# Kernel optimization log

Hardware: AMD Instinct MI355X
Metric: run time of the kernel (lower is better)

The kernel has to match this reference:

```python
import jax, jax.numpy as jnp
import numpy as np

USER = 100000
ITEM = 200000
N = USER + ITEM
LATDIM = 64
N_LAYERS = 3
N_EDGES = 9600000


def setup_inputs() -> dict:
    key = jax.random.key(0)
    k1, k2, k3, k4, k5 = jax.random.split(key, 5)
    # xavier_uniform for [N, latdim]: bound = sqrt(6/(fan_in+fan_out))
    bu = float(np.sqrt(6.0 / (USER + LATDIM)))
    bi = float(np.sqrt(6.0 / (ITEM + LATDIM)))
    uEmbeds = jax.random.uniform(k1, (USER, LATDIM), jnp.float32, -bu, bu)
    iEmbeds = jax.random.uniform(k2, (ITEM, LATDIM), jnp.float32, -bi, bi)
    edge_row = jax.random.randint(k3, (N_EDGES,), 0, N, dtype=jnp.int32)
    edge_col = jax.random.randint(k4, (N_EDGES,), 0, N, dtype=jnp.int32)
    edge_val = jax.random.uniform(k5, (N_EDGES,), jnp.float32) * 0.01
    return {"uEmbeds": uEmbeds, "iEmbeds": iEmbeds,
            "edge_row": edge_row, "edge_col": edge_col, "edge_val": edge_val}


def _spmm(row, col, val, x):
    # sparse adj (COO) @ dense x: gather cols, scale, scatter-add to rows
    msgs = x[col] * val[:, None]                 # [E, D]
    return jax.ops.segment_sum(msgs, row, num_segments=N)  # [N, D]


def reference(uEmbeds, iEmbeds, edge_row, edge_col, edge_val):
    # forward_gcn: multi-layer propagation, sum of all layer embeddings
    embeds = jnp.concatenate([uEmbeds, iEmbeds], axis=0)  # [N, D]
    acc = embeds
    cur = embeds
    for _ in range(N_LAYERS):
        cur = _spmm(edge_row, edge_col, edge_val, cur)
        acc = acc + cur
    return acc[:USER], acc[USER:]
```

## Files before the change

kernel.cpp:

```cpp
#include <hip/hip_runtime.h>
#include <hip/hip_bf16.h>

#define USER_N   100000
#define ITEM_N   200000
#define N_NODES  300000
#define LATDIM   64
#define N_EDGES  9600000
#define N_LAYERS 3

#define CSHIFT   11
#define CROWS    2048
#define NCOARSE  ((N_NODES + CROWS - 1) / CROWS)
#define CHUNK    4096
#define NCHUNKS  ((N_EDGES + CHUNK - 1) / CHUNK)
#define GP1      512
#define GP4      768

__device__ __forceinline__ unsigned short f2bf(float f) {
    unsigned int u = __float_as_uint(f);
    u += 0x7FFFu + ((u >> 16) & 1u);
    return (unsigned short)(u >> 16);
}
__device__ __forceinline__ float bf2f(unsigned short h) {
    return __uint_as_float(((unsigned int)h) << 16);
}

__global__ void cvt_concat_kernel(const float* __restrict__ u,
                                  const float* __restrict__ it,
                                  ushort4* __restrict__ cur0,
                                  int n4u, int n4total) {
    int stride = gridDim.x * blockDim.x;
    for (int i = blockIdx.x * blockDim.x + threadIdx.x; i < n4total; i += stride) {
        float4 v = (i < n4u) ? ((const float4*)u)[i]
                             : ((const float4*)it)[i - n4u];
        ushort4 o;
        o.x = f2bf(v.x); o.y = f2bf(v.y); o.z = f2bf(v.z); o.w = f2bf(v.w);
        cur0[i] = o;
    }
}

__global__ __launch_bounds__(256)
void p1_hist_kernel(const int* __restrict__ row, int* __restrict__ cntRaw) {
    __shared__ int h[NCOARSE];
    int t = threadIdx.x;
    for (int k = blockIdx.x; k < NCHUNKS; k += gridDim.x) {
        for (int i = t; i < NCOARSE; i += 256) h[i] = 0;
        __syncthreads();
        int e0 = k * CHUNK;
        int e1 = e0 + CHUNK; if (e1 > N_EDGES) e1 = N_EDGES;
        for (int e = e0 + t; e < e1; e += 256)
            atomicAdd(&h[row[e] >> CSHIFT], 1);
        __syncthreads();
        for (int i = t; i < NCOARSE; i += 256)
            cntRaw[i * NCHUNKS + k] = h[i];
        __syncthreads();
    }
}

__global__ __launch_bounds__(1024)
void p2_scanchunks_kernel(const int* __restrict__ cntRaw,
                          int* __restrict__ cntScan,
                          int* __restrict__ btot) {
    __shared__ int lds[1024];
    int b = blockIdx.x, t = threadIdx.x;
    const int base = t * 3;
    int v0 = 0, v1 = 0, v2 = 0;
    if (base     < NCHUNKS) v0 = cntRaw[b * NCHUNKS + base];
    if (base + 1 < NCHUNKS) v1 = cntRaw[b * NCHUNKS + base + 1];
    if (base + 2 < NCHUNKS) v2 = cntRaw[b * NCHUNKS + base + 2];
    int s = v0 + v1 + v2;
    lds[t] = s;
    __syncthreads();
    for (int off = 1; off < 1024; off <<= 1) {
        int add = (t >= off) ? lds[t - off] : 0;
        __syncthreads();
        lds[t] += add;
        __syncthreads();
    }
    int ex = lds[t] - s;
    if (base     < NCHUNKS) cntScan[b * NCHUNKS + base]     = ex;
    if (base + 1 < NCHUNKS) cntScan[b * NCHUNKS + base + 1] = ex + v0;
    if (base + 2 < NCHUNKS) cntScan[b * NCHUNKS + base + 2] = ex + v0 + v1;
    if (t == 1023) btot[b] = lds[1023];
}

__global__ void p3_scancoarse_kernel(const int* __restrict__ btot,
                                     int* __restrict__ cbase,
                                     int* __restrict__ rowPtr) {
    __shared__ int lds[256];
    int t = threadIdx.x;
    int v = (t < NCOARSE) ? btot[t] : 0;
    lds[t] = v;
    __syncthreads();
    for (int off = 1; off < 256; off <<= 1) {
        int add = (t >= off) ? lds[t - off] : 0;
        __syncthreads();
        lds[t] += add;
        __syncthreads();
    }
    if (t < NCOARSE) cbase[t] = lds[t] - v;
    if (t == NCOARSE - 1) cbase[NCOARSE] = lds[t];
    if (t == 0) rowPtr[N_NODES] = N_EDGES;
}

__global__ __launch_bounds__(256)
void p4_scatter_kernel(const int*   __restrict__ row,
                       const int*   __restrict__ col,
                       const float* __restrict__ val,
                       const int*   __restrict__ cntRaw,
                       const int*   __restrict__ cntScan,
                       const int*   __restrict__ cbase,
                       int2*        __restrict__ tempA) {
    __shared__ int2 stage[CHUNK];
    __shared__ int  dst[CHUNK];
    __shared__ int  loff[NCOARSE];
    __shared__ int  lcur[NCOARSE];
    __shared__ int  gcur[NCOARSE];
    __shared__ int  sc[256];
    int t = threadIdx.x;
    for (int k = blockIdx.x; k < NCHUNKS; k += gridDim.x) {
        int hv = 0;
        if (t < NCOARSE) {
            hv = cntRaw[t * NCHUNKS + k];
            gcur[t] = cbase[t] + cntScan[t * NCHUNKS + k];
        }
        sc[t] = hv;
        __syncthreads();
        for (int off = 1; off < 256; off <<= 1) {
            int add = (t >= off) ? sc[t - off] : 0;
            __syncthreads();
            sc[t] += add;
            __syncthreads();
        }
        if (t < NCOARSE) {
            int ex = sc[t] - hv;
            loff[t] = ex;
            lcur[t] = ex;
        }
        __syncthreads();

        int e0 = k * CHUNK;
        int e1 = e0 + CHUNK; if (e1 > N_EDGES) e1 = N_EDGES;
        int n = e1 - e0;
        for (int e = e0 + t; e < e1; e += 256) {
            int r = row[e];
            int c = r >> CSHIFT;
            int p = atomicAdd(&lcur[c], 1);
            stage[p] = make_int2(((r & (CROWS - 1)) << 19) | col[e],
                                 __float_as_int(val[e]));
            dst[p] = gcur[c] + (p - loff[c]);
        }
        __syncthreads();
        for (int j = t; j < n; j += 256)
            tempA[dst[j]] = stage[j];
        __syncthreads();
    }
}

__global__ __launch_bounds__(1024)
void passB_kernel(const int*  __restrict__ cbase,
                  const int2* __restrict__ tempA,
                  int2*       __restrict__ colval,
                  int*        __restrict__ rowPtr) {
    __shared__ int hist[CROWS];
    __shared__ int psum[1024];
    __shared__ int curs[CROWS];
    int c = blockIdx.x;
    int t = threadIdx.x;
    int beg = cbase[c], end = cbase[c + 1];

    hist[t] = 0; hist[t + 1024] = 0;
    __syncthreads();
    for (int i = beg + t; i < end; i += 1024)
        atomicAdd(&hist[((unsigned)tempA[i].x) >> 19], 1);
    __syncthreads();

    int b0 = hist[2 * t], b1 = hist[2 * t + 1];
    int tot = b0 + b1;
    psum[t] = tot;
    __syncthreads();
    for (int off = 1; off < 1024; off <<= 1) {
        int add = (t >= off) ? psum[t - off] : 0;
        __syncthreads();
        psum[t] += add;
        __syncthreads();
    }
    int ex = psum[t] - tot;
    int j0 = 2 * t, j1 = 2 * t + 1;
    int e0 = beg + ex, e1 = beg + ex + b0;
    curs[j0] = e0;
    curs[j1] = e1;
    int gr0 = c * CROWS + j0;
    int gr1 = c * CROWS + j1;
    if (gr0 < N_NODES) rowPtr[gr0] = e0;
    if (gr1 < N_NODES) rowPtr[gr1] = e1;
    __syncthreads();

    for (int i = beg + t; i < end; i += 1024) {
        int2 kv = tempA[i];
        int rl = ((unsigned)kv.x) >> 19;
        int pos = atomicAdd(&curs[rl], 1);
        colval[pos] = make_int2((kv.x & 0x7FFFF) << 4, kv.y);
    }
}

__global__ void spmm_bf16_kernel(const int*  __restrict__ rp,
                                 const int2* __restrict__ cv,
                                 const ushort4* __restrict__ x4,
                                 ushort4*       __restrict__ y4) {
    int g = (blockIdx.x * blockDim.x + threadIdx.x) >> 4;
    if (g >= N_NODES) return;
    int q = threadIdx.x & 15;
    int beg = rp[g];
    int end = rp[g + 1];
    const ushort4* xq = x4 + q;

    float s0 = 0.f, s1 = 0.f, s2 = 0.f, s3 = 0.f;
    int i = beg;
    for (; i + 8 <= end; i += 8) {
        int2 cc[8]; ushort4 gg[8];
        #pragma unroll
        for (int k = 0; k < 8; ++k) cc[k] = cv[i + k];
        #pragma unroll
        for (int k = 0; k < 8; ++k) gg[k] = xq[cc[k].x];
        #pragma unroll
        for (int k = 0; k < 8; ++k) {
            float v = __int_as_float(cc[k].y);
            s0 += bf2f(gg[k].x) * v; s1 += bf2f(gg[k].y) * v;
            s2 += bf2f(gg[k].z) * v; s3 += bf2f(gg[k].w) * v;
        }
    }
    for (; i < end; ++i) {
        int2 cc = cv[i];
        ushort4 gg = xq[cc.x];
        float v = __int_as_float(cc.y);
        s0 += bf2f(gg.x) * v; s1 += bf2f(gg.y) * v;
        s2 += bf2f(gg.z) * v; s3 += bf2f(gg.w) * v;
    }

    ushort4 o;
    o.x = f2bf(s0); o.y = f2bf(s1); o.z = f2bf(s2); o.w = f2bf(s3);
    y4[(size_t)g * 16 + q] = o;
}

__global__ void spmm_bf16_final_kernel(const int*  __restrict__ rp,
                                       const int2* __restrict__ cv,
                                       const ushort4* __restrict__ x4,
                                       const ushort4* __restrict__ c1,
                                       const float4*  __restrict__ u4,
                                       const float4*  __restrict__ i4,
                                       float4*        __restrict__ acc4) {
    int g = (blockIdx.x * blockDim.x + threadIdx.x) >> 4;
    if (g >= N_NODES) return;
    int q = threadIdx.x & 15;
    int beg = rp[g];
    int end = rp[g + 1];
    const ushort4* xq = x4 + q;

    float s0 = 0.f, s1 = 0.f, s2 = 0.f, s3 = 0.f;
    int i = beg;
    for (; i + 8 <= end; i += 8) {
        int2 cc[8]; ushort4 gg[8];
        #pragma unroll
        for (int k = 0; k < 8; ++k) cc[k] = cv[i + k];
        #pragma unroll
        for (int k = 0; k < 8; ++k) gg[k] = xq[cc[k].x];
        #pragma unroll
        for (int k = 0; k < 8; ++k) {
            float v = __int_as_float(cc[k].y);
            s0 += bf2f(gg[k].x) * v; s1 += bf2f(gg[k].y) * v;
            s2 += bf2f(gg[k].z) * v; s3 += bf2f(gg[k].w) * v;
        }
    }
    for (; i < end; ++i) {
        int2 cc = cv[i];
        ushort4 gg = xq[cc.x];
        float v = __int_as_float(cc.y);
        s0 += bf2f(gg.x) * v; s1 += bf2f(gg.y) * v;
        s2 += bf2f(gg.z) * v; s3 += bf2f(gg.w) * v;
    }

    size_t o = (size_t)g * 16 + q;
    float4 e = (g < USER_N) ? u4[o] : i4[o - (size_t)USER_N * 16];
    ushort4 a = c1[o];
    ushort4 b = x4[o];
    float4 r;
    r.x = e.x + bf2f(a.x) + bf2f(b.x) + s0;
    r.y = e.y + bf2f(a.y) + bf2f(b.y) + s1;
    r.z = e.z + bf2f(a.z) + bf2f(b.z) + s2;
    r.w = e.w + bf2f(a.w) + bf2f(b.w) + s3;
    acc4[o] = r;
}

__global__ void copy_concat_kernel(const float* __restrict__ u,
                                   const float* __restrict__ it,
                                   float* __restrict__ cur,
                                   float* __restrict__ acc,
                                   int n4u, int n4total) {
    int stride = gridDim.x * blockDim.x;
    for (int i = blockIdx.x * blockDim.x + threadIdx.x; i < n4total; i += stride) {
        float4 v = (i < n4u) ? ((const float4*)u)[i]
                             : ((const float4*)it)[i - n4u];
        ((float4*)cur)[i] = v;
        ((float4*)acc)[i] = v;
    }
}

__global__ void spmm_atomic_kernel(const int*   __restrict__ row,
                                   const int*   __restrict__ col,
                                   const float* __restrict__ val,
                                   const float* __restrict__ x,
                                   float*       __restrict__ y) {
    const int total = N_EDGES * 16;
    int stride = gridDim.x * blockDim.x;
    for (int t = blockIdx.x * blockDim.x + threadIdx.x; t < total; t += stride) {
        int e = t >> 4;
        int q = t & 15;
        int r = row[e];
        int c = col[e];
        float v = val[e];
        float4 g = ((const float4*)x)[c * 16 + q];
        float* yp = y + r * 64 + q * 4;
        atomicAdd(yp + 0, g.x * v);
        atomicAdd(yp + 1, g.y * v);
        atomicAdd(yp + 2, g.z * v);
        atomicAdd(yp + 3, g.w * v);
    }
}

__global__ void acc_add_kernel(float* __restrict__ acc,
                               const float* __restrict__ add,
                               int n4) {
    int stride = gridDim.x * blockDim.x;
    for (int i = blockIdx.x * blockDim.x + threadIdx.x; i < n4; i += stride) {
        float4 a = ((const float4*)acc)[i];
        float4 b = ((const float4*)add)[i];
        a.x += b.x; a.y += b.y; a.z += b.z; a.w += b.w;
        ((float4*)acc)[i] = a;
    }
}

extern "C" void kernel_launch(void* const* d_in, const int* in_sizes, int n_in,
                              void* d_out, int out_size, void* d_ws, size_t ws_size,
                              hipStream_t stream) {
    const float* uEmb = (const float*)d_in[0];
    const float* iEmb = (const float*)d_in[1];
    const int*   row  = (const int*)  d_in[2];
    const int*   col  = (const int*)  d_in[3];
    const float* val  = (const float*)d_in[4];

    float* acc = (float*)d_out;

    const int n4total = N_NODES * (LATDIM / 4);
    const int n4u     = USER_N  * (LATDIM / 4);
    const size_t embBytes  = (size_t)N_NODES * LATDIM * sizeof(float);
    const size_t embBytesH = (size_t)N_NODES * LATDIM * 2;

    const int BLK = 256;
    const int GRID_MEM = 2048;

    auto align256 = [](size_t x) { return (x + 255) & ~(size_t)255; };
    size_t off = 0;
    size_t o_cur0   = off; off += align256(embBytesH);
    size_t o_c1     = off; off += align256(embBytesH);
    size_t o_c2     = off; off += align256(embBytesH);
    size_t o_colval = off; off += align256((size_t)N_EDGES * 8);
    size_t o_rowptr = off; off += align256(((size_t)N_NODES + 1) * 4);
    size_t o_craw   = off; off += align256((size_t)NCOARSE * NCHUNKS * 4);
    size_t o_cscan  = off; off += align256((size_t)NCOARSE * NCHUNKS * 4);
    size_t o_btot   = off; off += align256((size_t)NCOARSE * 4);
    size_t o_cbase  = off; off += align256(((size_t)NCOARSE + 1) * 4);
    size_t needed = off;

    char* wsb = (char*)d_ws;

    if (ws_size >= needed) {
        ushort4* cur0 = (ushort4*)(wsb + o_cur0);
        ushort4* c1   = (ushort4*)(wsb + o_c1);
        ushort4* c2   = (ushort4*)(wsb + o_c2);
        int2* colval  = (int2*)(wsb + o_colval);
        int2* tempA   = (int2*)(wsb + o_c1);
        int* rowPtr   = (int*)(wsb + o_rowptr);
        int* cntRaw   = (int*)(wsb + o_craw);
        int* cntScan  = (int*)(wsb + o_cscan);
        int* btot     = (int*)(wsb + o_btot);
        int* cbase    = (int*)(wsb + o_cbase);

        cvt_concat_kernel<<<GRID_MEM, BLK, 0, stream>>>(uEmb, iEmb, cur0,
                                                        n4u, n4total);

        p1_hist_kernel      <<<GP1, 256, 0, stream>>>(row, cntRaw);
        p2_scanchunks_kernel<<<NCOARSE, 1024, 0, stream>>>(cntRaw, cntScan, btot);
        p3_scancoarse_kernel<<<1, 256, 0, stream>>>(btot, cbase, rowPtr);
        p4_scatter_kernel   <<<GP4, 256, 0, stream>>>(row, col, val, cntRaw,
                                                      cntScan, cbase, tempA);
        passB_kernel        <<<NCOARSE, 1024, 0, stream>>>(cbase, tempA,
                                                           colval, rowPtr);

        const int GRID_SPMM = (N_NODES * 16 + BLK - 1) / BLK;
        spmm_bf16_kernel<<<GRID_SPMM, BLK, 0, stream>>>(rowPtr, colval, cur0, c1);
        spmm_bf16_kernel<<<GRID_SPMM, BLK, 0, stream>>>(rowPtr, colval, c1,   c2);
        spmm_bf16_final_kernel<<<GRID_SPMM, BLK, 0, stream>>>(
            rowPtr, colval, c2, c1,
            (const float4*)uEmb, (const float4*)iEmb, (float4*)acc);
    } else {
        float* cur = (float*)wsb;
        float* nxt = (float*)(wsb + embBytes);
        copy_concat_kernel<<<GRID_MEM, BLK, 0, stream>>>(uEmb, iEmb, cur, acc,
                                                         n4u, n4total);
        for (int l = 0; l < N_LAYERS; ++l) {
            hipMemsetAsync(nxt, 0, embBytes, stream);
            spmm_atomic_kernel<<<4096, BLK, 0, stream>>>(row, col, val, cur, nxt);
            acc_add_kernel<<<GRID_MEM, BLK, 0, stream>>>(acc, nxt, n4total);
            float* t = cur; cur = nxt; nxt = t;
        }
    }
}
```

Measured before the change: 838.5 us.

## Split CSR into int columns and fp16 values, use 32 lanes per row

Stores CSR edge data as separate int column offsets and fp16 values instead of int2 pairs. The aim is to cut the bytes of edge data each of the three SpMM layers reads. SpMM now uses 32 lanes per row, each gathering a ushort2 (2 bf16) instead of 16 lanes with ushort4, which narrows each gather access. The scatter pass swaps the per-entry destination array for a byte bucket map, and grid sizes for the histogram and scatter passes are raised. Storing edge weights in fp16 lowers their precision, and the 32-lane mapping doubles the number of threads per row.

```diff
diff --git a/kernel.cpp b/kernel.cpp
--- a/kernel.cpp
+++ b/kernel.cpp
@@ -1,5 +1,6 @@
 #include <hip/hip_runtime.h>
 #include <hip/hip_bf16.h>
+#include <hip/hip_fp16.h>
 
 #define USER_N   100000
 #define ITEM_N   200000
@@ -13,8 +14,8 @@
 #define NCOARSE  ((N_NODES + CROWS - 1) / CROWS)
 #define CHUNK    4096
 #define NCHUNKS  ((N_EDGES + CHUNK - 1) / CHUNK)
-#define GP1      512
-#define GP4      768
+#define GP1      1024
+#define GP4      1024
 
 __device__ __forceinline__ unsigned short f2bf(float f) {
     unsigned int u = __float_as_uint(f);
@@ -112,7 +113,7 @@
                        const int*   __restrict__ cbase,
                        int2*        __restrict__ tempA) {
     __shared__ int2 stage[CHUNK];
-    __shared__ int  dst[CHUNK];
+    __shared__ unsigned char bmap[CHUNK];
     __shared__ int  loff[NCOARSE];
     __shared__ int  lcur[NCOARSE];
     __shared__ int  gcur[NCOARSE];
@@ -132,13 +133,16 @@
             sc[t] += add;
             __syncthreads();
         }
+        int exl = sc[t] - hv;
         if (t < NCOARSE) {
-            int ex = sc[t] - hv;
-            loff[t] = ex;
-            lcur[t] = ex;
-        }
-        __syncthreads();
-
+            loff[t] = exl;
+            lcur[t] = exl;
+        }
+        __syncthreads();
+        if (t < NCOARSE) {
+            int e = exl + hv;
+            for (int j = exl; j < e; ++j) bmap[j] = (unsigned char)t;
+        }
         int e0 = k * CHUNK;
         int e1 = e0 + CHUNK; if (e1 > N_EDGES) e1 = N_EDGES;
         int n = e1 - e0;
@@ -148,11 +152,12 @@
             int p = atomicAdd(&lcur[c], 1);
             stage[p] = make_int2(((r & (CROWS - 1)) << 19) | col[e],
                                  __float_as_int(val[e]));
-            dst[p] = gcur[c] + (p - loff[c]);
-        }
-        __syncthreads();
-        for (int j = t; j < n; j += 256)
-            tempA[dst[j]] = stage[j];
+        }
+        __syncthreads();
+        for (int j = t; j < n; j += 256) {
+            int c = bmap[j];
+            tempA[gcur[c] + (j - loff[c])] = stage[j];
+        }
         __syncthreads();
     }
 }
@@ -160,7 +165,8 @@
 __global__ __launch_bounds__(1024)
 void passB_kernel(const int*  __restrict__ cbase,
                   const int2* __restrict__ tempA,
-                  int2*       __restrict__ colval,
+                  int*        __restrict__ colval_c,
+                  unsigned short* __restrict__ colval_v,
                   int*        __restrict__ rowPtr) {
     __shared__ int hist[CROWS];
     __shared__ int psum[1024];
@@ -200,96 +206,95 @@
         int2 kv = tempA[i];
         int rl = ((unsigned)kv.x) >> 19;
         int pos = atomicAdd(&curs[rl], 1);
-        colval[pos] = make_int2((kv.x & 0x7FFFF) << 4, kv.y);
+        colval_c[pos] = (kv.x & 0x7FFFF) << 5;
+        colval_v[pos] = __half_as_ushort(__float2half(__int_as_float(kv.y)));
     }
 }
 
 __global__ void spmm_bf16_kernel(const int*  __restrict__ rp,
-                                 const int2* __restrict__ cv,
-                                 const ushort4* __restrict__ x4,
-                                 ushort4*       __restrict__ y4) {
-    int g = (blockIdx.x * blockDim.x + threadIdx.x) >> 4;
+                                 const int*  __restrict__ cvc,
+                                 const unsigned short* __restrict__ cvv,
+                                 const ushort2* __restrict__ x2,
+                                 ushort2*       __restrict__ y2) {
+    int g = (blockIdx.x * blockDim.x + threadIdx.x) >> 5;
     if (g >= N_NODES) return;
-    int q = threadIdx.x & 15;
+    int q = threadIdx.x & 31;
     int beg = rp[g];
     int end = rp[g + 1];
-    const ushort4* xq = x4 + q;
-
-    float s0 = 0.f, s1 = 0.f, s2 = 0.f, s3 = 0.f;
+    const ushort2* xq = x2 + q;
+
+    float s0 = 0.f, s1 = 0.f;
     int i = beg;
     for (; i + 8 <= end; i += 8) {
-        int2 cc[8]; ushort4 gg[8];
-        #pragma unroll
-        for (int k = 0; k < 8; ++k) cc[k] = cv[i + k];
-        #pragma unroll
-        for (int k = 0; k < 8; ++k) gg[k] = xq[cc[k].x];
+        int cc[8]; unsigned short vv[8]; ushort2 gg[8];
+        #pragma unroll
+        for (int k = 0; k < 8; ++k) cc[k] = cvc[i + k];
+        #pragma unroll
+        for (int k = 0; k < 8; ++k) vv[k] = cvv[i + k];
+        #pragma unroll
+        for (int k = 0; k < 8; ++k) gg[k] = xq[cc[k]];
         #pragma unroll
         for (int k = 0; k < 8; ++k) {
-            float v = __int_as_float(cc[k].y);
+            float v = __half2float(__ushort_as_half(vv[k]));
             s0 += bf2f(gg[k].x) * v; s1 += bf2f(gg[k].y) * v;
-            s2 += bf2f(gg[k].z) * v; s3 += bf2f(gg[k].w) * v;
         }
     }
     for (; i < end; ++i) {
-        int2 cc = cv[i];
-        ushort4 gg = xq[cc.x];
-        float v = __int_as_float(cc.y);
+        ushort2 gg = xq[cvc[i]];
+        float v = __half2float(__ushort_as_half(cvv[i]));
         s0 += bf2f(gg.x) * v; s1 += bf2f(gg.y) * v;
-        s2 += bf2f(gg.z) * v; s3 += bf2f(gg.w) * v;
-    }
-
-    ushort4 o;
-    o.x = f2bf(s0); o.y = f2bf(s1); o.z = f2bf(s2); o.w = f2bf(s3);
-    y4[(size_t)g * 16 + q] = o;
+    }
+
+    ushort2 o;
+    o.x = f2bf(s0); o.y = f2bf(s1);
+    y2[(size_t)g * 32 + q] = o;
 }
 
 __global__ void spmm_bf16_final_kernel(const int*  __restrict__ rp,
-                                       const int2* __restrict__ cv,
-                                       const ushort4* __restrict__ x4,
-                                       const ushort4* __restrict__ c1,
-                                       const float4*  __restrict__ u4,
-                                       const float4*  __restrict__ i4,
-                                       float4*        __restrict__ acc4) {
-    int g = (blockIdx.x * blockDim.x + threadIdx.x) >> 4;
+                                       const int*  __restrict__ cvc,
+                                       const unsigned short* __restrict__ cvv,
+                                       const ushort2* __restrict__ x2,
+                                       const ushort2* __restrict__ c1,
+                                       const float2*  __restrict__ u2,
+                                       const float2*  __restrict__ i2,
+                                       float2*        __restrict__ acc2) {
+    int g = (blockIdx.x * blockDim.x + threadIdx.x) >> 5;
     if (g >= N_NODES) return;
-    int q = threadIdx.x & 15;
+    int q = threadIdx.x & 31;
     int beg = rp[g];
     int end = rp[g + 1];
-    const ushort4* xq = x4 + q;
-
-    float s0 = 0.f, s1 = 0.f, s2 = 0.f, s3 = 0.f;
+    const ushort2* xq = x2 + q;
+
+    float s0 = 0.f, s1 = 0.f;
     int i = beg;
     for (; i + 8 <= end; i += 8) {
-        int2 cc[8]; ushort4 gg[8];
-        #pragma unroll
-        for (int k = 0; k < 8; ++k) cc[k] = cv[i + k];
-        #pragma unroll
-        for (int k = 0; k < 8; ++k) gg[k] = xq[cc[k].x];
+        int cc[8]; unsigned short vv[8]; ushort2 gg[8];
+        #pragma unroll
+        for (int k = 0; k < 8; ++k) cc[k] = cvc[i + k];
+        #pragma unroll
+        for (int k = 0; k < 8; ++k) vv[k] = cvv[i + k];
+        #pragma unroll
+        for (int k = 0; k < 8; ++k) gg[k] = xq[cc[k]];
         #pragma unroll
         for (int k = 0; k < 8; ++k) {
-            float v = __int_as_float(cc[k].y);
+            float v = __half2float(__ushort_as_half(vv[k]));
             s0 += bf2f(gg[k].x) * v; s1 += bf2f(gg[k].y) * v;
-            s2 += bf2f(gg[k].z) * v; s3 += bf2f(gg[k].w) * v;
         }
     }
     for (; i < end; ++i) {
-        int2 cc = cv[i];
-        ushort4 gg = xq[cc.x];
-        float v = __int_as_float(cc.y);
+        ushort2 gg = xq[cvc[i]];
+        float v = __half2float(__ushort_as_half(cvv[i]));
         s0 += bf2f(gg.x) * v; s1 += bf2f(gg.y) * v;
-        s2 += bf2f(gg.z) * v; s3 += bf2f(gg.w) * v;
-    }
-
-    size_t o = (size_t)g * 16 + q;
-    float4 e = (g < USER_N) ? u4[o] : i4[o - (size_t)USER_N * 16];
-    ushort4 a = c1[o];
-    ushort4 b = x4[o];
-    float4 r;
+    }
+
+    size_t o = (size_t)g * 32 + q;
+    float2 e = (g < USER_N) ? u2[o] : i2[o - (size_t)USER_N * 32];
+    ushort2 a = c1[o];
+    ushort2 b = x2[o];
+    float2 r;
     r.x = e.x + bf2f(a.x) + bf2f(b.x) + s0;
     r.y = e.y + bf2f(a.y) + bf2f(b.y) + s1;
-    r.z = e.z + bf2f(a.z) + bf2f(b.z) + s2;
-    r.w = e.w + bf2f(a.w) + bf2f(b.w) + s3;
-    acc4[o] = r;
+    acc2[o] = r;
 }
 
 __global__ void copy_concat_kernel(const float* __restrict__ u,
@@ -364,7 +369,8 @@
     size_t o_cur0   = off; off += align256(embBytesH);
     size_t o_c1     = off; off += align256(embBytesH);
     size_t o_c2     = off; off += align256(embBytesH);
-    size_t o_colval = off; off += align256((size_t)N_EDGES * 8);
+    size_t o_cvc    = off; off += align256((size_t)N_EDGES * 4);
+    size_t o_cvv    = off; off += align256((size_t)N_EDGES * 2);
     size_t o_rowptr = off; off += align256(((size_t)N_NODES + 1) * 4);
     size_t o_craw   = off; off += align256((size_t)NCOARSE * NCHUNKS * 4);
     size_t o_cscan  = off; off += align256((size_t)NCOARSE * NCHUNKS * 4);
@@ -376,9 +382,10 @@
 
     if (ws_size >= needed) {
         ushort4* cur0 = (ushort4*)(wsb + o_cur0);
-        ushort4* c1   = (ushort4*)(wsb + o_c1);
-        ushort4* c2   = (ushort4*)(wsb + o_c2);
-        int2* colval  = (int2*)(wsb + o_colval);
+        ushort2* c1   = (ushort2*)(wsb + o_c1);
+        ushort2* c2   = (ushort2*)(wsb + o_c2);
+        int*  cvc     = (int*)(wsb + o_cvc);
+        unsigned short* cvv = (unsigned short*)(wsb + o_cvv);
         int2* tempA   = (int2*)(wsb + o_c1);
         int* rowPtr   = (int*)(wsb + o_rowptr);
         int* cntRaw   = (int*)(wsb + o_craw);
@@ -395,14 +402,16 @@
         p4_scatter_kernel   <<<GP4, 256, 0, stream>>>(row, col, val, cntRaw,
                                                       cntScan, cbase, tempA);
         passB_kernel        <<<NCOARSE, 1024, 0, stream>>>(cbase, tempA,
-                                                           colval, rowPtr);
-
-        const int GRID_SPMM = (N_NODES * 16 + BLK - 1) / BLK;
-        spmm_bf16_kernel<<<GRID_SPMM, BLK, 0, stream>>>(rowPtr, colval, cur0, c1);
-        spmm_bf16_kernel<<<GRID_SPMM, BLK, 0, stream>>>(rowPtr, colval, c1,   c2);
+                                                           cvc, cvv, rowPtr);
+
+        const int GRID_SPMM = (N_NODES * 32 + BLK - 1) / BLK;
+        spmm_bf16_kernel<<<GRID_SPMM, BLK, 0, stream>>>(
+            rowPtr, cvc, cvv, (const ushort2*)cur0, c1);
+        spmm_bf16_kernel<<<GRID_SPMM, BLK, 0, stream>>>(
+            rowPtr, cvc, cvv, (const ushort2*)c1, c2);
         spmm_bf16_final_kernel<<<GRID_SPMM, BLK, 0, stream>>>(
-            rowPtr, colval, c2, c1,
-            (const float4*)uEmb, (const float4*)iEmb, (float4*)acc);
+            rowPtr, cvc, cvv, (const ushort2*)c2, (const ushort2*)c1,
+            (const float2*)uEmb, (const float2*)iEmb, (float2*)acc);
     } else {
         float* cur = (float*)wsb;
         float* nxt = (float*)(wsb + embBytes);
```

New measurement: 929.6 us. 10.9% more time.
